# Optimization experiments

Measured on AMD Instinct MI355X. Metric: run time of the kernel, lower is better.

Reference implementation:

```python
import jax, jax.numpy as jnp
import numpy as np

D_MODEL = 512
HEADS = 8

def setup_inputs() -> dict:
    key = jax.random.key(0)
    ks = jax.random.split(key, 11)
    B, S, D = 2, 4096, D_MODEL
    s = 1.0 / np.sqrt(D)
    inp = {
        'q': jax.random.normal(ks[0], (B, S, D), jnp.float32),
        'k': jax.random.normal(ks[1], (B, S, D), jnp.float32),
        'v': jax.random.normal(ks[2], (B, S, D), jnp.float32),
        'Wq': jax.random.normal(ks[3], (D, D), jnp.float32) * s,
        'bq': jnp.zeros((D,), jnp.float32),
        'Wk': jax.random.normal(ks[4], (D, D), jnp.float32) * s,
        'bk': jnp.zeros((D,), jnp.float32),
        'Wv': jax.random.normal(ks[5], (D, D), jnp.float32) * s,
        'bv': jnp.zeros((D,), jnp.float32),
        'Wo': jax.random.normal(ks[6], (D, D), jnp.float32) * s,
        'bo': jnp.zeros((D,), jnp.float32),
    }
    return inp

def _split_heads(x, h):
    B, S, D = x.shape
    return x.reshape(B, S, h, D // h).transpose(0, 2, 1, 3)  # [B,H,S,Dh]

def reference(q, k, v, Wq, bq, Wk, bk, Wv, bv, Wo, bo):
    # torch Linear: y = x @ W.T + b
    qh = _split_heads(q @ Wq.T + bq, HEADS)
    kh = _split_heads(k @ Wk.T + bk, HEADS)
    vh = _split_heads(v @ Wv.T + bv, HEADS)
    d_tensor = qh.shape[-1]
    scale = 1.0 / jnp.sqrt(jnp.asarray(d_tensor, qh.dtype))
    score = jnp.einsum('bhqd,bhkd->bhqk', qh, kh) * scale  # [B,H,S,S]
    attn = jax.nn.softmax(score, axis=-1)
    out = jnp.einsum('bhqk,bhkd->bhqd', attn, vh)
    B, H, S, Dh = out.shape
    out = out.transpose(0, 2, 1, 3).reshape(B, S, H * Dh)
    return out @ Wo.T + bo
```

## Files before the change

kernel.cpp:

```cpp
#include <hip/hip_runtime.h>

typedef short bf16x8 __attribute__((ext_vector_type(8)));
typedef float f32x4 __attribute__((ext_vector_type(4)));
typedef float f32x16 __attribute__((ext_vector_type(16)));
typedef unsigned short ushort_t;
typedef unsigned short us8 __attribute__((ext_vector_type(8)));
typedef unsigned short us4 __attribute__((ext_vector_type(4)));
typedef unsigned int u32x4 __attribute__((ext_vector_type(4)));
typedef unsigned int uint2v __attribute__((ext_vector_type(2)));

#define MFMA16(a, b, c) __builtin_amdgcn_mfma_f32_16x16x32_bf16((a), (b), (c), 0, 0, 0)
#define MFMA32(a, b, c) __builtin_amdgcn_mfma_f32_32x32x16_bf16((a), (b), (c), 0, 0, 0)

static __device__ __forceinline__ ushort_t f2bf(float f) {
    unsigned int u = __builtin_bit_cast(unsigned int, f);
    u += 0x7FFFu + ((u >> 16) & 1u);
    return (ushort_t)(u >> 16);
}

static __device__ __forceinline__ unsigned cvtpk(float lo, float hi) {
    unsigned r;
    asm("v_cvt_pk_bf16_f32 %0, %1, %2" : "=v"(r) : "v"(lo), "v"(hi));
    return r;
}

__global__ __launch_bounds__(256) void cvt_w(const float* __restrict__ W0,
                                             const float* __restrict__ W1,
                                             const float* __restrict__ W2,
                                             const float* __restrict__ W3,
                                             ushort_t* __restrict__ dst) {
    const float* src = (blockIdx.y == 0) ? W0 : (blockIdx.y == 1) ? W1
                     : (blockIdx.y == 2) ? W2 : W3;
    const int i = (blockIdx.x * 256 + threadIdx.x) * 8;
    float4 f0 = *(const float4*)(src + i);
    float4 f1 = *(const float4*)(src + i + 4);
    unsigned tw[4] = {cvtpk(f0.x, f0.y), cvtpk(f0.z, f0.w),
                      cvtpk(f1.x, f1.y), cvtpk(f1.z, f1.w)};
    *(u32x4*)(dst + (size_t)blockIdx.y * 262144 + i) = *(u32x4*)tw;
}

__global__ __launch_bounds__(256) void gemm_qkv(const float* __restrict__ qi,
                                                const float* __restrict__ ki,
                                                const float* __restrict__ vi,
                                                const ushort_t* __restrict__ Wball,
                                                const float* __restrict__ bq,
                                                const float* __restrict__ bk,
                                                const float* __restrict__ bv,
                                                ushort_t* __restrict__ Qh,
                                                ushort_t* __restrict__ Kh,
                                                ushort_t* __restrict__ Vt,
                                                float Cs) {
    constexpr int K = 512;
    __shared__ ushort_t As[64][72];
    __shared__ ushort_t Bs[64][72];

    const int which = blockIdx.y;
    const float*    Ap   = (which == 0) ? qi : (which == 1) ? ki : vi;
    const ushort_t* Wb   = Wball + (size_t)which * 262144;
    const float*    bias = (which == 0) ? bq : (which == 1) ? bk : bv;
    ushort_t*       outp = (which == 0) ? Qh : (which == 1) ? Kh : Vt;
    const float oscale   = (which == 0) ? Cs : 1.0f;

    int bid = blockIdx.x;
    bid = (bid & 7) * 128 + (bid >> 3);
    const int bm = bid >> 3;
    const int bn = bid & 7;
    const int m0 = bm * 64, n0 = bn * 64;
    const int t    = threadIdx.x;
    const int lane = t & 63;
    const int wv   = t >> 6;
    const int wm   = wv >> 1, wn = wv & 1;
    const int lrow = t >> 2;
    const int lcol = (t & 3) * 16;

    const int l15 = lane & 15;
    const int l16 = lane >> 4;

    f32x4 acc[2][2] = {};

    const float*    apf = Ap + (size_t)(m0 + lrow) * K + lcol;
    const ushort_t* bpb = Wb + (size_t)(n0 + lrow) * K + lcol;

    us8 br0, br1;
    f32x4 af[4];

    af[0] = *(const f32x4*)apf;       af[1] = *(const f32x4*)(apf + 4);
    af[2] = *(const f32x4*)(apf + 8); af[3] = *(const f32x4*)(apf + 12);
    br0 = *(const us8*)bpb; br1 = *(const us8*)(bpb + 8);

#pragma unroll 1
    for (int kt = 0; kt < K / 64; ++kt) {
        __syncthreads();
        {
            unsigned tw[8];
#pragma unroll
            for (int i = 0; i < 4; ++i) {
                tw[2 * i]     = cvtpk(af[i][0], af[i][1]);
                tw[2 * i + 1] = cvtpk(af[i][2], af[i][3]);
            }
            *(u32x4*)&As[lrow][lcol]     = *(u32x4*)tw;
            *(u32x4*)&As[lrow][lcol + 8] = *(u32x4*)(tw + 4);
        }
        *(us8*)&Bs[lrow][lcol]     = br0;
        *(us8*)&Bs[lrow][lcol + 8] = br1;
        __syncthreads();

        if (kt < K / 64 - 1) {
            const int off = (kt + 1) * 64;
            const float* s = apf + off;
            af[0] = *(const f32x4*)s;       af[1] = *(const f32x4*)(s + 4);
            af[2] = *(const f32x4*)(s + 8); af[3] = *(const f32x4*)(s + 12);
            br0 = *(const us8*)(bpb + off); br1 = *(const us8*)(bpb + off + 8);
        }

#pragma unroll
        for (int kk = 0; kk < 2; ++kk) {
            bf16x8 a0 = *(const bf16x8*)&As[wm * 32 + l15][kk * 32 + l16 * 8];
            bf16x8 a1 = *(const bf16x8*)&As[wm * 32 + 16 + l15][kk * 32 + l16 * 8];
            bf16x8 b0 = *(const bf16x8*)&Bs[wn * 32 + l15][kk * 32 + l16 * 8];
            bf16x8 b1 = *(const bf16x8*)&Bs[wn * 32 + 16 + l15][kk * 32 + l16 * 8];
            acc[0][0] = MFMA16(a0, b0, acc[0][0]);
            acc[0][1] = MFMA16(a0, b1, acc[0][1]);
            acc[1][0] = MFMA16(a1, b0, acc[1][0]);
            acc[1][1] = MFMA16(a1, b1, acc[1][1]);
        }
    }

#pragma unroll
    for (int i = 0; i < 2; ++i)
#pragma unroll
        for (int j = 0; j < 2; ++j) {
            const int n  = n0 + wn * 32 + j * 16 + l15;
            const float bv_ = bias[n];
            if (which == 2) {
                const int mbase = m0 + wm * 32 + i * 16 + l16 * 4;
                const int b = mbase >> 12, s = mbase & 4095;
                const int h = n >> 6, d = n & 63;
                ushort_t tmp[4];
#pragma unroll
                for (int v = 0; v < 4; ++v) tmp[v] = f2bf(acc[i][j][v] + bv_);
                *(us4*)(outp + (((size_t)(b * 8 + h)) * 64 + d) * 4096 + s) = *(us4*)tmp;
            } else {
#pragma unroll
                for (int v = 0; v < 4; ++v) {
                    const int m   = m0 + wm * 32 + i * 16 + l16 * 4 + v;
                    const int b = m >> 12, s = m & 4095;
                    const int h = n >> 6, d = n & 63;
                    outp[(((size_t)(b * 8 + h)) * 4096 + s) * 64 + d] =
                        f2bf((acc[i][j][v] + bv_) * oscale);
                }
            }
        }
}

__global__ __launch_bounds__(256) void gemm_out(const ushort_t* __restrict__ Ap,
                                                const ushort_t* __restrict__ Wb,
                                                const float* __restrict__ bias,
                                                float* __restrict__ outp) {
    constexpr int K = 512;
    __shared__ ushort_t As[64][72];
    __shared__ ushort_t Bs[64][72];

    int bid = blockIdx.x;
    bid = (bid & 7) * 128 + (bid >> 3);
    const int bm = bid >> 3;
    const int bn = bid & 7;
    const int m0 = bm * 64, n0 = bn * 64;
    const int t    = threadIdx.x;
    const int lane = t & 63;
    const int wv   = t >> 6;
    const int wm   = wv >> 1, wn = wv & 1;
    const int lrow = t >> 2;
    const int lcol = (t & 3) * 16;

    const int l15 = lane & 15;
    const int l16 = lane >> 4;

    f32x4 acc[2][2] = {};

    const ushort_t* apb = Ap + (size_t)(m0 + lrow) * K + lcol;
    const ushort_t* bpb = Wb + (size_t)(n0 + lrow) * K + lcol;

    us8 ar0, ar1, br0, br1;
    ar0 = *(const us8*)apb; ar1 = *(const us8*)(apb + 8);
    br0 = *(const us8*)bpb; br1 = *(const us8*)(bpb + 8);

#pragma unroll 1
    for (int kt = 0; kt < K / 64; ++kt) {
        __syncthreads();
        *(us8*)&As[lrow][lcol]     = ar0;
        *(us8*)&As[lrow][lcol + 8] = ar1;
        *(us8*)&Bs[lrow][lcol]     = br0;
        *(us8*)&Bs[lrow][lcol + 8] = br1;
        __syncthreads();

        if (kt < K / 64 - 1) {
            const int off = (kt + 1) * 64;
            ar0 = *(const us8*)(apb + off); ar1 = *(const us8*)(apb + off + 8);
            br0 = *(const us8*)(bpb + off); br1 = *(const us8*)(bpb + off + 8);
        }

#pragma unroll
        for (int kk = 0; kk < 2; ++kk) {
            bf16x8 a0 = *(const bf16x8*)&As[wm * 32 + l15][kk * 32 + l16 * 8];
            bf16x8 a1 = *(const bf16x8*)&As[wm * 32 + 16 + l15][kk * 32 + l16 * 8];
            bf16x8 b0 = *(const bf16x8*)&Bs[wn * 32 + l15][kk * 32 + l16 * 8];
            bf16x8 b1 = *(const bf16x8*)&Bs[wn * 32 + 16 + l15][kk * 32 + l16 * 8];
            acc[0][0] = MFMA16(a0, b0, acc[0][0]);
            acc[0][1] = MFMA16(a0, b1, acc[0][1]);
            acc[1][0] = MFMA16(a1, b0, acc[1][0]);
            acc[1][1] = MFMA16(a1, b1, acc[1][1]);
        }
    }

#pragma unroll
    for (int i = 0; i < 2; ++i)
#pragma unroll
        for (int j = 0; j < 2; ++j) {
            const int n  = n0 + wn * 32 + j * 16 + l15;
            const float bv_ = bias[n];
#pragma unroll
            for (int v = 0; v < 4; ++v) {
                const int m = m0 + wm * 32 + i * 16 + l16 * 4 + v;
                outp[(size_t)m * 512 + n] = acc[i][j][v] + bv_;
            }
        }
}

template <bool PARTIAL>
__global__ __launch_bounds__(256) void attn_fwd(const ushort_t* __restrict__ Qh,
                                                const ushort_t* __restrict__ Kh,
                                                const ushort_t* __restrict__ Vt,
                                                ushort_t* __restrict__ Out,
                                                float* __restrict__ Op,
                                                float* __restrict__ Lp) {
    constexpr int S = 4096;
    const int NT   = PARTIAL ? 32 : 64;
    const int half = PARTIAL ? blockIdx.z : 0;
    const int kt0  = half * 32;

    __shared__ __attribute__((aligned(16))) char KsB[2][8192];
    __shared__ __attribute__((aligned(16))) char VsB[2][8192];

    const int qt = blockIdx.x;
    const int bh = blockIdx.y;
    const int b  = bh >> 3, h = bh & 7;

    const int t    = threadIdx.x;
    const int lane = t & 63;
    const int wv   = t >> 6;
    const int l31  = lane & 31;
    const int hl   = lane >> 5;

    const int qw = qt * 128 + wv * 32;

    bf16x8 qf[4];
    {
        const ushort_t* qp = Qh + ((size_t)bh * S + qw + l31) * 64 + hl * 8;
#pragma unroll
        for (int ds = 0; ds < 4; ++ds) qf[ds] = *(const bf16x8*)(qp + ds * 16);
    }

    const f32x16 fzero = {};
    f32x16 accO[2] = {};
    float ll = 0.f;

    const int srow   = t >> 2;
    const int scolB  = (t & 3) * 32;
    const int swzrow = (srow & 7) << 4;

    const ushort_t* kgp = Kh + ((size_t)bh * S + kt0 * 64 + srow) * 64 + (t & 3) * 16;
    const ushort_t* vgp = Vt + ((size_t)bh * 64 + srow) * S + kt0 * 64 + (t & 3) * 16;

    us8 kr0, kr1, vr0, vr1;
#define LOADKV(i)                                                      \
    do {                                                               \
        const ushort_t* kn = kgp + (size_t)(i) * 4096;                 \
        const ushort_t* vn = vgp + (i) * 64;                           \
        kr0 = *(const us8*)kn; kr1 = *(const us8*)(kn + 8);            \
        vr0 = *(const us8*)vn; vr1 = *(const us8*)(vn + 8);            \
    } while (0)
#define STOREKV(buf)                                                   \
    do {                                                               \
        *(us8*)(KsB[buf] + srow * 128 + (scolB ^ swzrow))        = kr0;\
        *(us8*)(KsB[buf] + srow * 128 + ((scolB + 16) ^ swzrow)) = kr1;\
        *(us8*)(VsB[buf] + srow * 128 + (scolB ^ swzrow))        = vr0;\
        *(us8*)(VsB[buf] + srow * 128 + ((scolB + 16) ^ swzrow)) = vr1;\
    } while (0)

    LOADKV(0);
    STOREKV(0);
    LOADKV(1);
    __syncthreads();

#pragma unroll 1
    for (int kt = 0; kt < NT; ++kt) {
        const int cur = kt & 1;

        f32x16 sc[2];
        __builtin_amdgcn_s_setprio(1);
#pragma unroll
        for (int kb = 0; kb < 2; ++kb) {
            const int row = kb * 32 + l31;
            {
                bf16x8 kf = *(const bf16x8*)(KsB[cur] + row * 128 +
                               ((hl * 16) ^ ((row & 7) << 4)));
                sc[kb] = MFMA32(kf, qf[0], fzero);
            }
#pragma unroll
            for (int ds = 1; ds < 4; ++ds) {
                bf16x8 kf = *(const bf16x8*)(KsB[cur] + row * 128 +
                               ((ds * 32 + hl * 16) ^ ((row & 7) << 4)));
                sc[kb] = MFMA32(kf, qf[ds], sc[kb]);
            }
        }
        __builtin_amdgcn_s_setprio(0);

#pragma unroll
        for (int kb = 0; kb < 2; ++kb)
#pragma unroll
            for (int i = 0; i < 16; ++i)
                sc[kb][i] = __builtin_amdgcn_exp2f(sc[kb][i]);

        {
            f32x16 sv = sc[0] + sc[1];
            float s8[8];
#pragma unroll
            for (int i = 0; i < 8; ++i) s8[i] = sv[i] + sv[i + 8];
            ll += ((s8[0] + s8[1]) + (s8[2] + s8[3])) + ((s8[4] + s8[5]) + (s8[6] + s8[7]));
        }

        bf16x8 pb[4];
#pragma unroll
        for (int ks = 0; ks < 4; ++ks) {
            const int kb = ks >> 1, R0 = (ks & 1) * 8;
            unsigned w0 = cvtpk(sc[kb][R0 + 0], sc[kb][R0 + 1]);
            unsigned w1 = cvtpk(sc[kb][R0 + 2], sc[kb][R0 + 3]);
            unsigned w2 = cvtpk(sc[kb][R0 + 4], sc[kb][R0 + 5]);
            unsigned w3 = cvtpk(sc[kb][R0 + 6], sc[kb][R0 + 7]);
            uint2v s02 = __builtin_amdgcn_permlane32_swap(w0, w2, false, false);
            uint2v s13 = __builtin_amdgcn_permlane32_swap(w1, w3, false, false);
            u32x4 w = {s02.x, s13.x, s02.y, s13.y};
            pb[ks] = __builtin_bit_cast(bf16x8, w);
        }

        __builtin_amdgcn_s_setprio(1);
#pragma unroll
        for (int ks = 0; ks < 4; ++ks)
#pragma unroll
            for (int db = 0; db < 2; ++db) {
                const int row = db * 32 + l31;
                bf16x8 vf = *(const bf16x8*)(VsB[cur] + row * 128 +
                               ((ks * 32 + hl * 16) ^ ((row & 7) << 4)));
                accO[db] = MFMA32(vf, pb[ks], accO[db]);
            }
        __builtin_amdgcn_s_setprio(0);

        if (kt + 1 < NT) {
            STOREKV(cur ^ 1);
            if (kt + 2 < NT) LOADKV(kt + 2);
        }
        __syncthreads();
    }

    const float lt = ll + __shfl_xor(ll, 32);

    if constexpr (PARTIAL) {
        const size_t pb_ = (size_t)(half * 16 + bh) * 4096 + qw + l31;
        float* op = Op + pb_ * 64;
#pragma unroll
        for (int db = 0; db < 2; ++db)
#pragma unroll
            for (int q4 = 0; q4 < 4; ++q4) {
                float4 tmp = {accO[db][q4 * 4 + 0], accO[db][q4 * 4 + 1],
                              accO[db][q4 * 4 + 2], accO[db][q4 * 4 + 3]};
                *(float4*)(op + db * 32 + q4 * 8 + hl * 4) = tmp;
            }
        if (hl == 0) Lp[pb_] = lt;
    } else {
        const float inv = 1.0f / lt;
        ushort_t* orow = Out + ((size_t)b * S + qw + l31) * 512 + h * 64;
#pragma unroll
        for (int db = 0; db < 2; ++db)
#pragma unroll
            for (int q4 = 0; q4 < 4; ++q4) {
                unsigned w0 = cvtpk(accO[db][q4 * 4 + 0] * inv, accO[db][q4 * 4 + 1] * inv);
                unsigned w1 = cvtpk(accO[db][q4 * 4 + 2] * inv, accO[db][q4 * 4 + 3] * inv);
                unsigned tmp[2] = {w0, w1};
                *(us4*)(orow + db * 32 + q4 * 8 + hl * 4) = *(const us4*)tmp;
            }
    }
#undef LOADKV
#undef STOREKV
}

__global__ __launch_bounds__(256) void attn_merge(const float* __restrict__ Op,
                                                  const float* __restrict__ Lp,
                                                  ushort_t* __restrict__ Out) {
    const int bh = blockIdx.x;
    const int b  = bh >> 3, h = bh & 7;
    const int q  = blockIdx.y * 32 + (threadIdx.x >> 3);
    const int d0 = (threadIdx.x & 7) * 8;
    const size_t i0 = (size_t)bh * 4096 + q;
    const size_t i1 = i0 + 16 * 4096;
    const float inv = 1.0f / (Lp[i0] + Lp[i1]);
    const float* p0 = Op + i0 * 64 + d0;
    const float* p1 = Op + i1 * 64 + d0;
    f32x4 x0 = *(const f32x4*)p0, x1 = *(const f32x4*)(p0 + 4);
    f32x4 y0 = *(const f32x4*)p1, y1 = *(const f32x4*)(p1 + 4);
    unsigned tw[4];
    tw[0] = cvtpk((x0[0] + y0[0]) * inv, (x0[1] + y0[1]) * inv);
    tw[1] = cvtpk((x0[2] + y0[2]) * inv, (x0[3] + y0[3]) * inv);
    tw[2] = cvtpk((x1[0] + y1[0]) * inv, (x1[1] + y1[1]) * inv);
    tw[3] = cvtpk((x1[2] + y1[2]) * inv, (x1[3] + y1[3]) * inv);
    *(u32x4*)(Out + ((size_t)b * 4096 + q) * 512 + h * 64 + d0) = *(u32x4*)tw;
}

extern "C" void kernel_launch(void* const* d_in, const int* in_sizes, int n_in,
                              void* d_out, int out_size, void* d_ws, size_t ws_size,
                              hipStream_t stream) {
    const float* q  = (const float*)d_in[0];
    const float* k  = (const float*)d_in[1];
    const float* v  = (const float*)d_in[2];
    const float* Wq = (const float*)d_in[3];
    const float* bq = (const float*)d_in[4];
    const float* bk = (const float*)d_in[6];
    const float* bv = (const float*)d_in[8];
    const float* bo = (const float*)d_in[10];

    char* w = (char*)d_ws;
    const size_t SZ     = (size_t)2 * 8 * 4096 * 64 * 2;
    const size_t OFF_WB = 4 * SZ;
    const size_t OFF_OP = OFF_WB + 2 * 1024 * 1024;
    const size_t OFF_LP = OFF_OP + (size_t)2 * 16 * 4096 * 64 * 4;
    const size_t TOTAL  = OFF_LP + (size_t)2 * 16 * 4096 * 4;

    ushort_t* Qh  = (ushort_t*)(w);
    ushort_t* Kh  = (ushort_t*)(w + SZ);
    ushort_t* Vtr = (ushort_t*)(w + 2 * SZ);
    ushort_t* AO  = (ushort_t*)(w + 3 * SZ);
    ushort_t* Wb  = (ushort_t*)(w + OFF_WB);
    float*    Opr = (float*)(w + OFF_OP);
    float*    Lpr = (float*)(w + OFF_LP);

    const bool split = ws_size >= TOTAL;

    cvt_w<<<dim3(128, 4), 256, 0, stream>>>(Wq, (const float*)d_in[5],
                                            (const float*)d_in[7], (const float*)d_in[9], Wb);

    const float Cs = 0.125f * 1.44269504f;
    gemm_qkv<<<dim3(1024, 3), 256, 0, stream>>>(q, k, v, Wb, bq, bk, bv, Qh, Kh, Vtr, Cs);

    if (split) {
        attn_fwd<true><<<dim3(32, 16, 2), 256, 0, stream>>>(Qh, Kh, Vtr, AO, Opr, Lpr);
        attn_merge<<<dim3(16, 128), 256, 0, stream>>>(Opr, Lpr, AO);
    } else {
        attn_fwd<false><<<dim3(32, 16), 256, 0, stream>>>(Qh, Kh, Vtr, AO, nullptr, nullptr);
    }

    gemm_out<<<1024, 256, 0, stream>>>(AO, Wb + 3 * 262144, bo, (float*)d_out);
}
```

Before: 158.4 us.

## Pre-swizzle K/V tiles in projection and stream them via direct global-to-LDS loads

The QKV projection now writes K and V in a tile-contiguous layout that is already XOR-swizzled in 64-key blocks. That lets the attention kernel copy each K/V tile straight into LDS with global_load_lds, skipping the register staging and the separate LDS stores. The attention loop is unrolled by two with compile-time buffer indices. The split-K variant and its merge kernel are removed, so only 512 attention blocks run, which may underfill the GPU. Scattered 2-byte stores in the projection epilogue may also raise its cost.

```diff
diff --git a/kernel.cpp b/kernel.cpp
--- a/kernel.cpp
+++ b/kernel.cpp
@@ -12,6 +12,8 @@
 #define MFMA16(a, b, c) __builtin_amdgcn_mfma_f32_16x16x32_bf16((a), (b), (c), 0, 0, 0)
 #define MFMA32(a, b, c) __builtin_amdgcn_mfma_f32_32x32x16_bf16((a), (b), (c), 0, 0, 0)
 
+template <int N> struct ic { static constexpr int value = N; };
+
 static __device__ __forceinline__ ushort_t f2bf(float f) {
     unsigned int u = __builtin_bit_cast(unsigned int, f);
     u += 0x7FFFu + ((u >> 16) & 1u);
@@ -22,6 +24,13 @@
     unsigned r;
     asm("v_cvt_pk_bf16_f32 %0, %1, %2" : "=v"(r) : "v"(lo), "v"(hi));
     return r;
+}
+
+static __device__ __forceinline__ void gload16(const void* g, void* l) {
+    __builtin_amdgcn_global_load_lds(
+        (const __attribute__((address_space(1))) unsigned int*)g,
+        (__attribute__((address_space(3))) unsigned int*)l,
+        16, 0, 0);
 }
 
 __global__ __launch_bounds__(256) void cvt_w(const float* __restrict__ W0,
@@ -59,7 +68,6 @@
     const ushort_t* Wb   = Wball + (size_t)which * 262144;
     const float*    bias = (which == 0) ? bq : (which == 1) ? bk : bv;
     ushort_t*       outp = (which == 0) ? Qh : (which == 1) ? Kh : Vt;
-    const float oscale   = (which == 0) ? Cs : 1.0f;
 
     int bid = blockIdx.x;
     bid = (bid & 7) * 128 + (bid >> 3);
@@ -132,22 +140,34 @@
         for (int j = 0; j < 2; ++j) {
             const int n  = n0 + wn * 32 + j * 16 + l15;
             const float bv_ = bias[n];
+            const int h = n >> 6, d = n & 63;
             if (which == 2) {
                 const int mbase = m0 + wm * 32 + i * 16 + l16 * 4;
-                const int b = mbase >> 12, s = mbase & 4095;
-                const int h = n >> 6, d = n & 63;
+                const int b = mbase >> 12, key = mbase & 4095;
+                const int kr = key & 63;
+                const int o  = (kr & 7) | ((((kr >> 3) ^ d) & 7) << 3);
                 ushort_t tmp[4];
 #pragma unroll
                 for (int v = 0; v < 4; ++v) tmp[v] = f2bf(acc[i][j][v] + bv_);
-                *(us4*)(outp + (((size_t)(b * 8 + h)) * 64 + d) * 4096 + s) = *(us4*)tmp;
+                *(us4*)(outp + (size_t)(b * 8 + h) * 262144 +
+                        (size_t)(key >> 6) * 4096 + d * 64 + o) = *(us4*)tmp;
+            } else if (which == 1) {
+#pragma unroll
+                for (int v = 0; v < 4; ++v) {
+                    const int m = m0 + wm * 32 + i * 16 + l16 * 4 + v;
+                    const int b = m >> 12, s = m & 4095;
+                    const int row = s & 63;
+                    const int o   = (d & 7) | ((((d >> 3) ^ row) & 7) << 3);
+                    outp[(size_t)(b * 8 + h) * 262144 + (size_t)(s >> 6) * 4096 +
+                         row * 64 + o] = f2bf(acc[i][j][v] + bv_);
+                }
             } else {
 #pragma unroll
                 for (int v = 0; v < 4; ++v) {
-                    const int m   = m0 + wm * 32 + i * 16 + l16 * 4 + v;
+                    const int m = m0 + wm * 32 + i * 16 + l16 * 4 + v;
                     const int b = m >> 12, s = m & 4095;
-                    const int h = n >> 6, d = n & 63;
                     outp[(((size_t)(b * 8 + h)) * 4096 + s) * 64 + d] =
-                        f2bf((acc[i][j][v] + bv_) * oscale);
+                        f2bf((acc[i][j][v] + bv_) * Cs);
                 }
             }
         }
@@ -227,20 +247,13 @@
         }
 }
 
-template <bool PARTIAL>
 __global__ __launch_bounds__(256) void attn_fwd(const ushort_t* __restrict__ Qh,
-                                                const ushort_t* __restrict__ Kh,
-                                                const ushort_t* __restrict__ Vt,
-                                                ushort_t* __restrict__ Out,
-                                                float* __restrict__ Op,
-                                                float* __restrict__ Lp) {
-    constexpr int S = 4096;
-    const int NT   = PARTIAL ? 32 : 64;
-    const int half = PARTIAL ? blockIdx.z : 0;
-    const int kt0  = half * 32;
-
-    __shared__ __attribute__((aligned(16))) char KsB[2][8192];
-    __shared__ __attribute__((aligned(16))) char VsB[2][8192];
+                                                const ushort_t* __restrict__ Kg,
+                                                const ushort_t* __restrict__ Vg,
+                                                ushort_t* __restrict__ Out) {
+    constexpr int S  = 4096;
+    constexpr int NT = 64;
+    __shared__ __attribute__((aligned(16))) char LDS[32768];
 
     const int qt = blockIdx.x;
     const int bh = blockIdx.y;
@@ -265,65 +278,58 @@
     f32x16 accO[2] = {};
     float ll = 0.f;
 
-    const int srow   = t >> 2;
-    const int scolB  = (t & 3) * 32;
-    const int swzrow = (srow & 7) << 4;
-
-    const ushort_t* kgp = Kh + ((size_t)bh * S + kt0 * 64 + srow) * 64 + (t & 3) * 16;
-    const ushort_t* vgp = Vt + ((size_t)bh * 64 + srow) * S + kt0 * 64 + (t & 3) * 16;
-
-    us8 kr0, kr1, vr0, vr1;
-#define LOADKV(i)                                                      \
-    do {                                                               \
-        const ushort_t* kn = kgp + (size_t)(i) * 4096;                 \
-        const ushort_t* vn = vgp + (i) * 64;                           \
-        kr0 = *(const us8*)kn; kr1 = *(const us8*)(kn + 8);            \
-        vr0 = *(const us8*)vn; vr1 = *(const us8*)(vn + 8);            \
-    } while (0)
-#define STOREKV(buf)                                                   \
-    do {                                                               \
-        *(us8*)(KsB[buf] + srow * 128 + (scolB ^ swzrow))        = kr0;\
-        *(us8*)(KsB[buf] + srow * 128 + ((scolB + 16) ^ swzrow)) = kr1;\
-        *(us8*)(VsB[buf] + srow * 128 + (scolB ^ swzrow))        = vr0;\
-        *(us8*)(VsB[buf] + srow * 128 + ((scolB + 16) ^ swzrow)) = vr1;\
-    } while (0)
-
-    LOADKV(0);
-    STOREKV(0);
-    LOADKV(1);
-    __syncthreads();
-
-#pragma unroll 1
-    for (int kt = 0; kt < NT; ++kt) {
-        const int cur = kt & 1;
-
-        f32x16 sc[2];
+    int gofs[4];
+#pragma unroll
+    for (int j = 0; j < 4; ++j)
+        gofs[j] = l31 * 128 + ((j * 32 + hl * 16) ^ ((l31 & 7) << 4));
+
+    const int wvb = wv * 1024;
+    const ushort_t* kg = Kg + (size_t)bh * 262144 + wv * 512 + lane * 8;
+    const ushort_t* vg = Vg + (size_t)bh * 262144 + wv * 512 + lane * 8;
+
+    auto issue = [&](int kt, auto curc) {
+        constexpr int CUR = decltype(curc)::value;
+        const ushort_t* kg_ = kg + (size_t)kt * 4096;
+        const ushort_t* vg_ = vg + (size_t)kt * 4096;
+        gload16(kg_,        LDS + CUR * 8192 + wvb);
+        gload16(kg_ + 2048, LDS + CUR * 8192 + 4096 + wvb);
+        gload16(vg_,        LDS + 16384 + CUR * 8192 + wvb);
+        gload16(vg_ + 2048, LDS + 16384 + CUR * 8192 + 4096 + wvb);
+    };
+
+    auto tile = [&](int kt, auto curc) {
+        constexpr int CUR = decltype(curc)::value;
+
+        f32x16 sc0, sc1;
         __builtin_amdgcn_s_setprio(1);
-#pragma unroll
-        for (int kb = 0; kb < 2; ++kb) {
-            const int row = kb * 32 + l31;
-            {
-                bf16x8 kf = *(const bf16x8*)(KsB[cur] + row * 128 +
-                               ((hl * 16) ^ ((row & 7) << 4)));
-                sc[kb] = MFMA32(kf, qf[0], fzero);
-            }
-#pragma unroll
-            for (int ds = 1; ds < 4; ++ds) {
-                bf16x8 kf = *(const bf16x8*)(KsB[cur] + row * 128 +
-                               ((ds * 32 + hl * 16) ^ ((row & 7) << 4)));
-                sc[kb] = MFMA32(kf, qf[ds], sc[kb]);
-            }
+        {
+            bf16x8 kf = *(const bf16x8*)(LDS + CUR * 8192 + gofs[0]);
+            sc0 = MFMA32(kf, qf[0], fzero);
+        }
+#pragma unroll
+        for (int ds = 1; ds < 4; ++ds) {
+            bf16x8 kf = *(const bf16x8*)(LDS + CUR * 8192 + gofs[ds]);
+            sc0 = MFMA32(kf, qf[ds], sc0);
+        }
+        {
+            bf16x8 kf = *(const bf16x8*)(LDS + CUR * 8192 + 4096 + gofs[0]);
+            sc1 = MFMA32(kf, qf[0], fzero);
+        }
+#pragma unroll
+        for (int ds = 1; ds < 4; ++ds) {
+            bf16x8 kf = *(const bf16x8*)(LDS + CUR * 8192 + 4096 + gofs[ds]);
+            sc1 = MFMA32(kf, qf[ds], sc1);
         }
         __builtin_amdgcn_s_setprio(0);
 
 #pragma unroll
-        for (int kb = 0; kb < 2; ++kb)
-#pragma unroll
-            for (int i = 0; i < 16; ++i)
-                sc[kb][i] = __builtin_amdgcn_exp2f(sc[kb][i]);
+        for (int i = 0; i < 16; ++i) {
+            sc0[i] = __builtin_amdgcn_exp2f(sc0[i]);
+            sc1[i] = __builtin_amdgcn_exp2f(sc1[i]);
+        }
 
         {
-            f32x16 sv = sc[0] + sc[1];
+            f32x16 sv = sc0 + sc1;
             float s8[8];
 #pragma unroll
             for (int i = 0; i < 8; ++i) s8[i] = sv[i] + sv[i + 8];
@@ -333,11 +339,19 @@
         bf16x8 pb[4];
 #pragma unroll
         for (int ks = 0; ks < 4; ++ks) {
-            const int kb = ks >> 1, R0 = (ks & 1) * 8;
-            unsigned w0 = cvtpk(sc[kb][R0 + 0], sc[kb][R0 + 1]);
-            unsigned w1 = cvtpk(sc[kb][R0 + 2], sc[kb][R0 + 3]);
-            unsigned w2 = cvtpk(sc[kb][R0 + 4], sc[kb][R0 + 5]);
-            unsigned w3 = cvtpk(sc[kb][R0 + 6], sc[kb][R0 + 7]);
+            const int R0 = (ks & 1) * 8;
+            float e0, e1, e2, e3, e4, e5, e6, e7;
+            if (ks < 2) {
+                e0 = sc0[R0+0]; e1 = sc0[R0+1]; e2 = sc0[R0+2]; e3 = sc0[R0+3];
+                e4 = sc0[R0+4]; e5 = sc0[R0+5]; e6 = sc0[R0+6]; e7 = sc0[R0+7];
+            } else {
+                e0 = sc1[R0+0]; e1 = sc1[R0+1]; e2 = sc1[R0+2]; e3 = sc1[R0+3];
+                e4 = sc1[R0+4]; e5 = sc1[R0+5]; e6 = sc1[R0+6]; e7 = sc1[R0+7];
+            }
+            unsigned w0 = cvtpk(e0, e1);
+            unsigned w1 = cvtpk(e2, e3);
+            unsigned w2 = cvtpk(e4, e5);
+            unsigned w3 = cvtpk(e6, e7);
             uint2v s02 = __builtin_amdgcn_permlane32_swap(w0, w2, false, false);
             uint2v s13 = __builtin_amdgcn_permlane32_swap(w1, w3, false, false);
             u32x4 w = {s02.x, s13.x, s02.y, s13.y};
@@ -346,74 +360,44 @@
 
         __builtin_amdgcn_s_setprio(1);
 #pragma unroll
-        for (int ks = 0; ks < 4; ++ks)
-#pragma unroll
-            for (int db = 0; db < 2; ++db) {
-                const int row = db * 32 + l31;
-                bf16x8 vf = *(const bf16x8*)(VsB[cur] + row * 128 +
-                               ((ks * 32 + hl * 16) ^ ((row & 7) << 4)));
-                accO[db] = MFMA32(vf, pb[ks], accO[db]);
-            }
+        for (int ks = 0; ks < 4; ++ks) {
+            {
+                bf16x8 vf = *(const bf16x8*)(LDS + 16384 + CUR * 8192 + gofs[ks]);
+                accO[0] = MFMA32(vf, pb[ks], accO[0]);
+            }
+            {
+                bf16x8 vf = *(const bf16x8*)(LDS + 16384 + CUR * 8192 + 4096 + gofs[ks]);
+                accO[1] = MFMA32(vf, pb[ks], accO[1]);
+            }
+        }
         __builtin_amdgcn_s_setprio(0);
 
-        if (kt + 1 < NT) {
-            STOREKV(cur ^ 1);
-            if (kt + 2 < NT) LOADKV(kt + 2);
-        }
         __syncthreads();
+        if (kt + 2 < NT) issue(kt + 2, curc);
+    };
+
+    issue(0, ic<0>{});
+    issue(1, ic<1>{});
+    __syncthreads();
+
+#pragma unroll 1
+    for (int kt2 = 0; kt2 < NT; kt2 += 2) {
+        tile(kt2,     ic<0>{});
+        tile(kt2 + 1, ic<1>{});
     }
 
-    const float lt = ll + __shfl_xor(ll, 32);
-
-    if constexpr (PARTIAL) {
-        const size_t pb_ = (size_t)(half * 16 + bh) * 4096 + qw + l31;
-        float* op = Op + pb_ * 64;
-#pragma unroll
-        for (int db = 0; db < 2; ++db)
-#pragma unroll
-            for (int q4 = 0; q4 < 4; ++q4) {
-                float4 tmp = {accO[db][q4 * 4 + 0], accO[db][q4 * 4 + 1],
-                              accO[db][q4 * 4 + 2], accO[db][q4 * 4 + 3]};
-                *(float4*)(op + db * 32 + q4 * 8 + hl * 4) = tmp;
-            }
-        if (hl == 0) Lp[pb_] = lt;
-    } else {
-        const float inv = 1.0f / lt;
-        ushort_t* orow = Out + ((size_t)b * S + qw + l31) * 512 + h * 64;
-#pragma unroll
-        for (int db = 0; db < 2; ++db)
-#pragma unroll
-            for (int q4 = 0; q4 < 4; ++q4) {
-                unsigned w0 = cvtpk(accO[db][q4 * 4 + 0] * inv, accO[db][q4 * 4 + 1] * inv);
-                unsigned w1 = cvtpk(accO[db][q4 * 4 + 2] * inv, accO[db][q4 * 4 + 3] * inv);
-                unsigned tmp[2] = {w0, w1};
-                *(us4*)(orow + db * 32 + q4 * 8 + hl * 4) = *(const us4*)tmp;
-            }
-    }
-#undef LOADKV
-#undef STOREKV
-}
-
-__global__ __launch_bounds__(256) void attn_merge(const float* __restrict__ Op,
-                                                  const float* __restrict__ Lp,
-                                                  ushort_t* __restrict__ Out) {
-    const int bh = blockIdx.x;
-    const int b  = bh >> 3, h = bh & 7;
-    const int q  = blockIdx.y * 32 + (threadIdx.x >> 3);
-    const int d0 = (threadIdx.x & 7) * 8;
-    const size_t i0 = (size_t)bh * 4096 + q;
-    const size_t i1 = i0 + 16 * 4096;
-    const float inv = 1.0f / (Lp[i0] + Lp[i1]);
-    const float* p0 = Op + i0 * 64 + d0;
-    const float* p1 = Op + i1 * 64 + d0;
-    f32x4 x0 = *(const f32x4*)p0, x1 = *(const f32x4*)(p0 + 4);
-    f32x4 y0 = *(const f32x4*)p1, y1 = *(const f32x4*)(p1 + 4);
-    unsigned tw[4];
-    tw[0] = cvtpk((x0[0] + y0[0]) * inv, (x0[1] + y0[1]) * inv);
-    tw[1] = cvtpk((x0[2] + y0[2]) * inv, (x0[3] + y0[3]) * inv);
-    tw[2] = cvtpk((x1[0] + y1[0]) * inv, (x1[1] + y1[1]) * inv);
-    tw[3] = cvtpk((x1[2] + y1[2]) * inv, (x1[3] + y1[3]) * inv);
-    *(u32x4*)(Out + ((size_t)b * 4096 + q) * 512 + h * 64 + d0) = *(u32x4*)tw;
+    const float lt  = ll + __shfl_xor(ll, 32);
+    const float inv = 1.0f / lt;
+    ushort_t* orow = Out + ((size_t)b * S + qw + l31) * 512 + h * 64;
+#pragma unroll
+    for (int db = 0; db < 2; ++db)
+#pragma unroll
+        for (int q4 = 0; q4 < 4; ++q4) {
+            unsigned w0 = cvtpk(accO[db][q4 * 4 + 0] * inv, accO[db][q4 * 4 + 1] * inv);
+            unsigned w1 = cvtpk(accO[db][q4 * 4 + 2] * inv, accO[db][q4 * 4 + 3] * inv);
+            unsigned tmp[2] = {w0, w1};
+            *(us4*)(orow + db * 32 + q4 * 8 + hl * 4) = *(const us4*)tmp;
+        }
 }
 
 extern "C" void kernel_launch(void* const* d_in, const int* in_sizes, int n_in,
@@ -429,21 +413,13 @@
     const float* bo = (const float*)d_in[10];
 
     char* w = (char*)d_ws;
-    const size_t SZ     = (size_t)2 * 8 * 4096 * 64 * 2;
-    const size_t OFF_WB = 4 * SZ;
-    const size_t OFF_OP = OFF_WB + 2 * 1024 * 1024;
-    const size_t OFF_LP = OFF_OP + (size_t)2 * 16 * 4096 * 64 * 4;
-    const size_t TOTAL  = OFF_LP + (size_t)2 * 16 * 4096 * 4;
+    const size_t SZ = (size_t)2 * 8 * 4096 * 64 * 2;
 
     ushort_t* Qh  = (ushort_t*)(w);
     ushort_t* Kh  = (ushort_t*)(w + SZ);
     ushort_t* Vtr = (ushort_t*)(w + 2 * SZ);
     ushort_t* AO  = (ushort_t*)(w + 3 * SZ);
-    ushort_t* Wb  = (ushort_t*)(w + OFF_WB);
-    float*    Opr = (float*)(w + OFF_OP);
-    float*    Lpr = (float*)(w + OFF_LP);
-
-    const bool split = ws_size >= TOTAL;
+    ushort_t* Wb  = (ushort_t*)(w + 4 * SZ);
 
     cvt_w<<<dim3(128, 4), 256, 0, stream>>>(Wq, (const float*)d_in[5],
                                             (const float*)d_in[7], (const float*)d_in[9], Wb);
@@ -451,12 +427,7 @@
     const float Cs = 0.125f * 1.44269504f;
     gemm_qkv<<<dim3(1024, 3), 256, 0, stream>>>(q, k, v, Wb, bq, bk, bv, Qh, Kh, Vtr, Cs);
 
-    if (split) {
-        attn_fwd<true><<<dim3(32, 16, 2), 256, 0, stream>>>(Qh, Kh, Vtr, AO, Opr, Lpr);
-        attn_merge<<<dim3(16, 128), 256, 0, stream>>>(Opr, Lpr, AO);
-    } else {
-        attn_fwd<false><<<dim3(32, 16), 256, 0, stream>>>(Qh, Kh, Vtr, AO, nullptr, nullptr);
-    }
+    attn_fwd<<<dim3(32, 16), 256, 0, stream>>>(Qh, Kh, Vtr, AO);
 
     gemm_out<<<1024, 256, 0, stream>>>(AO, Wb + 3 * 262144, bo, (float*)d_out);
 }
```

Result: faster. 142.1 us (-10.3%).
